# Optimization experiments

Hardware: AMD Instinct MI355X
Metric: run time of the kernel (lower is better)

Reference implementation:

```python
import jax, jax.numpy as jnp
import numpy as np


def _min_gru_layer(h_in, Wz, bz, Wh, bh):
    # h_in: [B, T, D_in]; gates/candidate via two GEMMs
    z = jax.nn.sigmoid(jnp.einsum('btd,dh->bth', h_in, Wz) + bz)  # [B,T,H]
    h_tilde = jnp.einsum('btd,dh->bth', h_in, Wh) + bh            # [B,T,H]
    # Recurrence h_t = a_t * h_{t-1} + b_t with a_t = 1-z_t, b_t = z_t*h_tilde.
    # h_0 = 0 (frozen zeros param in the torch module), so the associative
    # scan over (a, b) directly yields h_t for t = 1..T.
    a = 1.0 - z
    b = z * h_tilde

    def combine(c1, c2):
        a1, b1 = c1
        a2, b2 = c2
        return a1 * a2, a2 * b1 + b2

    _, h = jax.lax.associative_scan(combine, (a, b), axis=1)
    return h


def setup_inputs() -> dict:
    key = jax.random.key(0)
    ks = jax.random.split(key, 8)
    B, T, Din, H, Dout = 8, 4096, 512, 1024, 512
    s_in = 1.0 / np.sqrt(Din)
    s_h = 1.0 / np.sqrt(H)
    return {
        'x':   jax.random.normal(ks[0], (B, T, Din), dtype=jnp.float32),
        'Wz0': jax.random.normal(ks[1], (Din, H), dtype=jnp.float32) * s_in,
        'bz0': jnp.zeros((H,), dtype=jnp.float32),
        'Wh0': jax.random.normal(ks[2], (Din, H), dtype=jnp.float32) * s_in,
        'bh0': jnp.zeros((H,), dtype=jnp.float32),
        'Wz1': jax.random.normal(ks[3], (H, H), dtype=jnp.float32) * s_h,
        'bz1': jnp.zeros((H,), dtype=jnp.float32),
        'Wh1': jax.random.normal(ks[4], (H, H), dtype=jnp.float32) * s_h,
        'bh1': jnp.zeros((H,), dtype=jnp.float32),
        'Wfc': jax.random.normal(ks[5], (H, Dout), dtype=jnp.float32) * s_h,
        'bfc': jnp.zeros((Dout,), dtype=jnp.float32),
    }


def reference(x, Wz0, bz0, Wh0, bh0, Wz1, bz1, Wh1, bh1, Wfc, bfc):
    h = _min_gru_layer(x, Wz0, bz0, Wh0, bh0)   # layer 0
    h = _min_gru_layer(h, Wz1, bz1, Wh1, bh1)   # layer 1
    return jnp.einsum('bth,ho->bto', h, Wfc) + bfc
```

## Files before the change

### kernel.cpp

```cpp
#include <hip/hip_runtime.h>

typedef __attribute__((ext_vector_type(4))) float fv4;
typedef __attribute__((ext_vector_type(8))) _Float16 hv8;
typedef __attribute__((ext_vector_type(4))) _Float16 hv4;
typedef __attribute__((ext_vector_type(2))) _Float16 hv2;

__device__ __forceinline__ void gload16(const void* g, void* l) {
  __builtin_amdgcn_global_load_lds(
      (const __attribute__((address_space(1))) unsigned int*)g,
      (__attribute__((address_space(3))) unsigned int*)l, 16, 0, 0);
}

struct GemmCore256 {
  const _Float16 *ap, *bp;
  size_t rstep;
  _Float16* ls;
  const _Float16 *fa, *fb;
  int wv;

  __device__ __forceinline__ void init(const _Float16* A, const _Float16* Bt,
                                       _Float16* lds, int m0, int n0, int K,
                                       int tid) {
    ls = lds;
    wv = tid >> 6;
    const int lane = tid & 63;
    const int wm = wv >> 2, wn = wv & 3;
    const int quad = lane >> 4, r = lane & 15;
    const int cg = (tid & 3) ^ ((tid >> 3) & 3);
    ap = A  + (size_t)(m0 + (tid >> 2)) * K + cg * 8;
    bp = Bt + (size_t)(n0 + (tid >> 2)) * K + cg * 8;
    rstep = (size_t)128 * K;
    const int sq = quad ^ ((r >> 1) & 3);
    fa = ls + (wm * 128 + r) * 32 + sq * 8;
    fb = ls + 8192 + (wn * 64 + r) * 32 + sq * 8;
  }

  __device__ __forceinline__ void stage(int s) {
    _Float16* d = ls + (s & 3) * 16384 + wv * 512;
    const _Float16* a = ap + (size_t)s * 32;
    const _Float16* b = bp + (size_t)s * 32;
    gload16(a,         d);
    gload16(a + rstep, d + 4096);
    gload16(b,         d + 8192);
    gload16(b + rstep, d + 12288);
  }

  template <int VM>
  __device__ __forceinline__ void body(fv4 acc[8][4], int s) {
    asm volatile("s_waitcnt vmcnt(%0)" :: "n"(VM) : "memory");
    __builtin_amdgcn_s_barrier();
    __builtin_amdgcn_sched_barrier(0);
    const _Float16* fA = fa + (s & 3) * 16384;
    const _Float16* fB = fb + (s & 3) * 16384;
    hv8 a0[4], b0[4], a1[4];
#pragma unroll
    for (int t = 0; t < 4; ++t) a0[t] = *(const hv8*)(fA + t * 512);
#pragma unroll
    for (int t = 0; t < 4; ++t) b0[t] = *(const hv8*)(fB + t * 512);
#pragma unroll
    for (int t = 0; t < 4; ++t) a1[t] = *(const hv8*)(fA + (t + 4) * 512);
    __builtin_amdgcn_s_setprio(1);
#pragma unroll
    for (int tm = 0; tm < 4; ++tm)
#pragma unroll
      for (int tn = 0; tn < 4; ++tn)
        acc[tm][tn] = __builtin_amdgcn_mfma_f32_16x16x32_f16(a0[tm], b0[tn],
                                                             acc[tm][tn], 0, 0, 0);
#pragma unroll
    for (int tm = 0; tm < 4; ++tm)
#pragma unroll
      for (int tn = 0; tn < 4; ++tn)
        acc[tm + 4][tn] = __builtin_amdgcn_mfma_f32_16x16x32_f16(a1[tm], b0[tn],
                                                                 acc[tm + 4][tn], 0, 0, 0);
    __builtin_amdgcn_s_setprio(0);
    asm volatile("s_waitcnt lgkmcnt(0)" ::: "memory");
    __builtin_amdgcn_sched_barrier(0);
    __builtin_amdgcn_s_barrier();
  }

  __device__ __forceinline__ void run(fv4 acc[8][4], int K) {
    const int ns = K >> 5;
    stage(0); stage(1); stage(2);
    int s = 0;
    for (; s < ns - 3; ++s) { stage(s + 3); body<12>(acc, s); }
    body<8>(acc, s); ++s;
    body<4>(acc, s); ++s;
    body<0>(acc, s);
  }
};

__device__ __forceinline__ void xcd_map(int bid, int ntl2, int mt_per_x,
                                        int& m0, int& n0) {
  const int xcd = bid & 7;
  const int k2  = bid >> 3;
  m0 = (xcd * mt_per_x + (k2 >> ntl2)) * 256;
  n0 = (k2 & ((1 << ntl2) - 1)) * 256;
}

__global__ __launch_bounds__(512)
void gemm_gate(const _Float16* __restrict__ A, const _Float16* __restrict__ Btf,
               _Float16* __restrict__ zh2,
               float* __restrict__ cA, float* __restrict__ cB,
               const float* __restrict__ bz, const float* __restrict__ bh,
               int K, int ntl2, int mt_per_x) {
  __shared__ _Float16 lds[4 * 16384];
  const int tid  = threadIdx.x;
  const int lane = tid & 63;
  const int wave = tid >> 6;
  const int wm = wave >> 2, wn = wave & 3;
  const int quad = lane >> 4, r = lane & 15;
  int m0, n0;
  xcd_map(blockIdx.x, ntl2, mt_per_x, m0, n0);

  GemmCore256 core;
  core.init(A, Btf, lds, m0, n0, K, tid);
  fv4 acc[8][4] = {};
  core.run(acc, K);

  const int jb   = (n0 + wn * 64) >> 1;
  const int row0 = m0 + wm * 128 + quad * 4;
  const int cb   = (m0 >> 6) + wm * 2;
#pragma unroll
  for (int tn = 0; tn < 2; ++tn) {
    const int j = jb + tn * 16 + r;
    const float bzv = bz[j];
    const float bhv = bh[j];
#pragma unroll
    for (int tg = 0; tg < 2; ++tg) {
      float qA[4], qB[4];
#pragma unroll
      for (int tq = 0; tq < 4; ++tq) {
        const int tm = tg * 4 + tq;
        float sA = 1.0f, sB = 0.0f;
#pragma unroll
        for (int r2 = 0; r2 < 4; ++r2) {
          const float zpre = acc[tm][tn][r2] + bzv;
          const float hpre = acc[tm][tn + 2][r2] + bhv;
          const float z = 1.0f / (1.0f + __expf(-zpre));
          const _Float16 a16 = (_Float16)(1.0f - z);
          const _Float16 b16 = (_Float16)(z * hpre);
          hv2 ab = {a16, b16};
          *(hv2*)(zh2 + ((size_t)(row0 + tm * 16 + r2) * 1024 + j) * 2) = ab;
          const float af = (float)a16, bf = (float)b16;
          sB = af * sB + bf;
          sA = sA * af;
        }
        qA[tq] = sA; qB[tq] = sB;
      }
#pragma unroll
      for (int tq = 0; tq < 4; ++tq) {
        float Av = qA[tq], Bv = qB[tq];
        float Ap = __shfl_up(Av, 16, 64);
        float Bp = __shfl_up(Bv, 16, 64);
        if (quad >= 1) { Bv = Av * Bp + Bv; Av = Ap * Av; }
        Ap = __shfl_up(Av, 32, 64);
        Bp = __shfl_up(Bv, 32, 64);
        if (quad >= 2) { Bv = Av * Bp + Bv; Av = Ap * Av; }
        qA[tq] = Av; qB[tq] = Bv;
      }
      if (quad == 3) {
        float CA = 1.0f, CB = 0.0f;
#pragma unroll
        for (int tq = 0; tq < 4; ++tq) { CB = qA[tq] * CB + qB[tq]; CA *= qA[tq]; }
        cA[(size_t)(cb + tg) * 1024 + j] = CA;
        cB[(size_t)(cb + tg) * 1024 + j] = CB;
      }
    }
  }
}

__global__ __launch_bounds__(512)
void gemm_f16_bt(const _Float16* __restrict__ A, const _Float16* __restrict__ Bt,
                 float* __restrict__ C, const float* __restrict__ bias,
                 int N, int K, int ntl2, int mt_per_x) {
  __shared__ _Float16 lds[4 * 16384];
  const int tid  = threadIdx.x;
  const int lane = tid & 63;
  const int wave = tid >> 6;
  const int wm = wave >> 2, wn = wave & 3;
  const int quad = lane >> 4, r = lane & 15;
  int m0, n0;
  xcd_map(blockIdx.x, ntl2, mt_per_x, m0, n0);

  GemmCore256 core;
  core.init(A, Bt, lds, m0, n0, K, tid);
  fv4 acc[8][4] = {};
  core.run(acc, K);

  const int col0 = n0 + wn * 64 + r;
  const int row0 = m0 + wm * 128 + quad * 4;
#pragma unroll
  for (int tn = 0; tn < 4; ++tn) {
    const int col = col0 + tn * 16;
    const float bs = bias[col];
#pragma unroll
    for (int tm = 0; tm < 8; ++tm) {
#pragma unroll
      for (int r2 = 0; r2 < 4; ++r2) {
        C[(size_t)(row0 + tm * 16 + r2) * N + col] = acc[tm][tn][r2] + bs;
      }
    }
  }
}

__global__ void cvt_f16(const float* __restrict__ x, _Float16* __restrict__ y) {
  size_t i = ((size_t)blockIdx.x * 256 + threadIdx.x) * 4;
  fv4 v = *(const fv4*)(x + i);
  *(hv4*)(y + i) = __builtin_convertvector(v, hv4);
}

__global__ void transpose_cvt(const float* __restrict__ W, _Float16* __restrict__ Wt,
                              int K, int N, int mult, int off) {
  __shared__ float tile[32][33];
  const int tx = threadIdx.x, ty = threadIdx.y;
  const int n  = blockIdx.x * 32 + tx;
  const int kb = blockIdx.y * 32;
  for (int i = ty; i < 32; i += 8)
    tile[i][tx] = W[(size_t)(kb + i) * N + n];
  __syncthreads();
  const int k = kb + tx;
  for (int i = ty; i < 32; i += 8)
    Wt[(size_t)(blockIdx.x * mult + off + i) * K + k] = (_Float16)tile[tx][i];
}

__global__ void scan_phaseB(const float* __restrict__ cA, const float* __restrict__ cB,
                            float* __restrict__ hcy) {
  const int gtid = blockIdx.x * 256 + threadIdx.x;
  const int lane = gtid & 63;
  const int wid  = gtid >> 6;
  const int h  = (wid & 255) * 4;
  const int bb = wid >> 8;
  const size_t o = (size_t)(bb * 64 + lane) * 1024 + h;
  fv4 Aa = *(const fv4*)(cA + o);
  fv4 Bv = *(const fv4*)(cB + o);
#pragma unroll
  for (int d = 1; d < 64; d <<= 1) {
    fv4 Ap, Bp;
#pragma unroll
    for (int k = 0; k < 4; ++k) {
      Ap[k] = __shfl_up(Aa[k], d, 64);
      Bp[k] = __shfl_up(Bv[k], d, 64);
    }
    if (lane >= d) {
      Bv = Aa * Bp + Bv;
      Aa = Ap * Aa;
    }
  }
  fv4 hc;
#pragma unroll
  for (int k = 0; k < 4; ++k) hc[k] = __shfl_up(Bv[k], 1, 64);
  if (lane == 0) { hc.x = 0.f; hc.y = 0.f; hc.z = 0.f; hc.w = 0.f; }
  *(fv4*)(hcy + o) = hc;
}

__global__ void scan_phaseC(const _Float16* __restrict__ zh2,
                            const float* __restrict__ hcy,
                            _Float16* __restrict__ hout) {
  const int idx = blockIdx.x * 256 + threadIdx.x;
  const int h  = (idx & 255) * 4;
  const int c  = (idx >> 8) & 63;
  const int bb = idx >> 14;
  const size_t base = ((size_t)(bb * 4096 + c * 64) * 1024 + h) * 2;
  const size_t ob   = (size_t)(bb * 4096 + c * 64) * 1024 + h;
  const size_t o    = (size_t)(bb * 64 + c) * 1024 + h;
  fv4 hc = *(const fv4*)(hcy + o);
#pragma unroll 4
  for (int t = 0; t < 64; ++t) {
    hv8 v = *(const hv8*)(zh2 + base + (size_t)t * 2048);
    fv4 av = __builtin_convertvector(__builtin_shufflevector(v, v, 0, 2, 4, 6), fv4);
    fv4 bv = __builtin_convertvector(__builtin_shufflevector(v, v, 1, 3, 5, 7), fv4);
    hc = av * hc + bv;
    *(hv4*)(hout + ob + (size_t)t * 1024) = __builtin_convertvector(hc, hv4);
  }
}

extern "C" void kernel_launch(void* const* d_in, const int* in_sizes, int n_in,
                              void* d_out, int out_size, void* d_ws, size_t ws_size,
                              hipStream_t stream) {
  const float* x   = (const float*)d_in[0];
  const float* Wz0 = (const float*)d_in[1];
  const float* bz0 = (const float*)d_in[2];
  const float* Wh0 = (const float*)d_in[3];
  const float* bh0 = (const float*)d_in[4];
  const float* Wz1 = (const float*)d_in[5];
  const float* bz1 = (const float*)d_in[6];
  const float* Wh1 = (const float*)d_in[7];
  const float* bh1 = (const float*)d_in[8];
  const float* Wfc = (const float*)d_in[9];
  const float* bfc = (const float*)d_in[10];

  const int Mrows = 32768;
  const int H = 1024, Din = 512, Dout = 512;

  char* w = (char*)d_ws;
  _Float16* zh2   = (_Float16*)w; w += (size_t)Mrows * 2 * H * 2;
  _Float16* hx    = (_Float16*)w; w += (size_t)Mrows * H * 2;
  _Float16* Wzh0t = (_Float16*)w; w += (size_t)2 * H * Din * 2;
  _Float16* Wzh1t = (_Float16*)w; w += (size_t)2 * H * H * 2;
  _Float16* Wft   = (_Float16*)w; w += (size_t)Dout * H * 2;
  float*    cA    = (float*)w;    w += (size_t)8 * 64 * H * 4;
  float*    cB    = (float*)w;    w += (size_t)8 * 64 * H * 4;
  float*    hcy   = (float*)w;    w += (size_t)8 * 64 * H * 4;
  _Float16* Xb    = hx;

  cvt_f16<<<Mrows * Din / 1024, 256, 0, stream>>>(x, Xb);
  transpose_cvt<<<dim3(H / 32, Din / 32), dim3(32, 8), 0, stream>>>(Wz0, Wzh0t, Din, H, 64, 0);
  transpose_cvt<<<dim3(H / 32, Din / 32), dim3(32, 8), 0, stream>>>(Wh0, Wzh0t, Din, H, 64, 32);
  transpose_cvt<<<dim3(H / 32, H / 32),   dim3(32, 8), 0, stream>>>(Wz1, Wzh1t, H, H, 64, 0);
  transpose_cvt<<<dim3(H / 32, H / 32),   dim3(32, 8), 0, stream>>>(Wh1, Wzh1t, H, H, 64, 32);
  transpose_cvt<<<dim3(Dout / 32, H / 32), dim3(32, 8), 0, stream>>>(Wfc, Wft, H, Dout, 32, 0);

  gemm_gate<<<1024, 512, 0, stream>>>(Xb, Wzh0t, zh2, cA, cB, bz0, bh0, Din, 3, 16);
  scan_phaseB<<<512, 256, 0, stream>>>(cA, cB, hcy);
  scan_phaseC<<<512, 256, 0, stream>>>(zh2, hcy, hx);

  gemm_gate<<<1024, 512, 0, stream>>>(hx, Wzh1t, zh2, cA, cB, bz1, bh1, H, 3, 16);
  scan_phaseB<<<512, 256, 0, stream>>>(cA, cB, hcy);
  scan_phaseC<<<512, 256, 0, stream>>>(zh2, hcy, hx);

  gemm_f16_bt<<<256, 512, 0, stream>>>(hx, Wft, (float*)d_out, bfc, Dout, H, 1, 16);
}
```

Measured before the change: 506.6 us.

## Split GEMM main loop into two phases with interleaved A/B staging

The per-stage GEMM body is split into two half-phases. Each half reads its LDS fragments, issues global-to-LDS loads for one operand (A or B) of stage s+3, then runs 16 MFMAs, with a barrier and lgkmcnt wait between them. The aim is to spread global loads and LDS reads across the MFMA work and shorten barrier stalls. Both GEMM kernels also get launch_bounds(512, 2) to ask for two blocks per CU. That caps register use while each thread already holds 128 fp32 accumulators, so spills are likely. The 128 KB LDS buffer per block may also stop a second block from fitting at all.

```diff
diff --git a/kernel.cpp b/kernel.cpp
--- a/kernel.cpp
+++ b/kernel.cpp
@@ -35,7 +35,7 @@
     fb = ls + 8192 + (wn * 64 + r) * 32 + sq * 8;
   }
 
-  __device__ __forceinline__ void stage(int s) {
+  __device__ __forceinline__ void stage4(int s) {
     _Float16* d = ls + (s & 3) * 16384 + wv * 512;
     const _Float16* a = ap + (size_t)s * 32;
     const _Float16* b = bp + (size_t)s * 32;
@@ -44,21 +44,33 @@
     gload16(b,         d + 8192);
     gload16(b + rstep, d + 12288);
   }
-
-  template <int VM>
-  __device__ __forceinline__ void body(fv4 acc[8][4], int s) {
-    asm volatile("s_waitcnt vmcnt(%0)" :: "n"(VM) : "memory");
-    __builtin_amdgcn_s_barrier();
-    __builtin_amdgcn_sched_barrier(0);
+  __device__ __forceinline__ void stageA(int s) {
+    _Float16* d = ls + (s & 3) * 16384 + wv * 512;
+    const _Float16* a = ap + (size_t)s * 32;
+    gload16(a,         d);
+    gload16(a + rstep, d + 4096);
+  }
+  __device__ __forceinline__ void stageB(int s) {
+    _Float16* d = ls + (s & 3) * 16384 + wv * 512;
+    const _Float16* b = bp + (size_t)s * 32;
+    gload16(b,         d + 8192);
+    gload16(b + rstep, d + 12288);
+  }
+
+  template <bool STAGE>
+  __device__ __forceinline__ void phaseA(fv4 acc[8][4], hv8 b0[4], int s) {
     const _Float16* fA = fa + (s & 3) * 16384;
     const _Float16* fB = fb + (s & 3) * 16384;
-    hv8 a0[4], b0[4], a1[4];
+    hv8 a0[4];
 #pragma unroll
     for (int t = 0; t < 4; ++t) a0[t] = *(const hv8*)(fA + t * 512);
 #pragma unroll
     for (int t = 0; t < 4; ++t) b0[t] = *(const hv8*)(fB + t * 512);
-#pragma unroll
-    for (int t = 0; t < 4; ++t) a1[t] = *(const hv8*)(fA + (t + 4) * 512);
+    if (STAGE) stageA(s + 3);
+    __builtin_amdgcn_sched_barrier(0);
+    __builtin_amdgcn_s_barrier();
+    asm volatile("s_waitcnt lgkmcnt(0)" ::: "memory");
+    __builtin_amdgcn_sched_barrier(0);
     __builtin_amdgcn_s_setprio(1);
 #pragma unroll
     for (int tm = 0; tm < 4; ++tm)
@@ -66,6 +78,25 @@
       for (int tn = 0; tn < 4; ++tn)
         acc[tm][tn] = __builtin_amdgcn_mfma_f32_16x16x32_f16(a0[tm], b0[tn],
                                                              acc[tm][tn], 0, 0, 0);
+    __builtin_amdgcn_s_setprio(0);
+    __builtin_amdgcn_sched_barrier(0);
+    __builtin_amdgcn_s_barrier();
+  }
+
+  template <int VM, bool STAGE>
+  __device__ __forceinline__ void phaseB(fv4 acc[8][4], hv8 b0[4], int s) {
+    const _Float16* fA = fa + (s & 3) * 16384;
+    hv8 a1[4];
+#pragma unroll
+    for (int t = 0; t < 4; ++t) a1[t] = *(const hv8*)(fA + (t + 4) * 512);
+    if (STAGE) stageB(s + 3);
+    if constexpr (VM >= 0)
+      asm volatile("s_waitcnt vmcnt(%0)" :: "n"(VM) : "memory");
+    __builtin_amdgcn_sched_barrier(0);
+    __builtin_amdgcn_s_barrier();
+    asm volatile("s_waitcnt lgkmcnt(0)" ::: "memory");
+    __builtin_amdgcn_sched_barrier(0);
+    __builtin_amdgcn_s_setprio(1);
 #pragma unroll
     for (int tm = 0; tm < 4; ++tm)
 #pragma unroll
@@ -73,19 +104,24 @@
         acc[tm + 4][tn] = __builtin_amdgcn_mfma_f32_16x16x32_f16(a1[tm], b0[tn],
                                                                  acc[tm + 4][tn], 0, 0, 0);
     __builtin_amdgcn_s_setprio(0);
-    asm volatile("s_waitcnt lgkmcnt(0)" ::: "memory");
     __builtin_amdgcn_sched_barrier(0);
     __builtin_amdgcn_s_barrier();
   }
 
   __device__ __forceinline__ void run(fv4 acc[8][4], int K) {
     const int ns = K >> 5;
-    stage(0); stage(1); stage(2);
+    stage4(0); stage4(1); stage4(2);
+    asm volatile("s_waitcnt vmcnt(8)" ::: "memory");
+    __builtin_amdgcn_s_barrier();
     int s = 0;
-    for (; s < ns - 3; ++s) { stage(s + 3); body<12>(acc, s); }
-    body<8>(acc, s); ++s;
-    body<4>(acc, s); ++s;
-    body<0>(acc, s);
+    for (; s < ns - 3; ++s) {
+      hv8 b0[4];
+      phaseA<true>(acc, b0, s);
+      phaseB<8, true>(acc, b0, s);
+    }
+    { hv8 b0[4]; phaseA<false>(acc, b0, s); phaseB<4, false>(acc, b0, s); } ++s;
+    { hv8 b0[4]; phaseA<false>(acc, b0, s); phaseB<0, false>(acc, b0, s); } ++s;
+    { hv8 b0[4]; phaseA<false>(acc, b0, s); phaseB<-1, false>(acc, b0, s); }
   }
 };
 
@@ -97,7 +133,7 @@
   n0 = (k2 & ((1 << ntl2) - 1)) * 256;
 }
 
-__global__ __launch_bounds__(512)
+__global__ __launch_bounds__(512, 2)
 void gemm_gate(const _Float16* __restrict__ A, const _Float16* __restrict__ Btf,
                _Float16* __restrict__ zh2,
                float* __restrict__ cA, float* __restrict__ cB,
@@ -169,7 +205,7 @@
   }
 }
 
-__global__ __launch_bounds__(512)
+__global__ __launch_bounds__(512, 2)
 void gemm_f16_bt(const _Float16* __restrict__ A, const _Float16* __restrict__ Bt,
                  float* __restrict__ C, const float* __restrict__ bias,
                  int N, int K, int ntl2, int mt_per_x) {
```

Measured after the change: 517.2 us. 1.02x slower.

## Restructure GEMM main loop to one barrier per k-step and add occupancy bound

Applied to the files above, without the earlier changes.

The k-loop of the shared GEMM core now uses a single workgroup barrier per step instead of two. The next stage's global-to-LDS loads are issued right after that barrier, and the vmcnt wait moves to the end of the step. The trailing lgkmcnt wait and second barrier are dropped, so waves can move into the next step sooner and load issue overlaps more with MFMA work. Both GEMM kernels also get __launch_bounds__(512, 2), which caps registers per thread. With a 128-float accumulator per thread, that cap risks spills, and the 128 KB LDS footprint per block may stop two blocks from ever sharing a CU.

```diff
diff --git a/kernel.cpp b/kernel.cpp
--- a/kernel.cpp
+++ b/kernel.cpp
@@ -35,7 +35,7 @@
     fb = ls + 8192 + (wn * 64 + r) * 32 + sq * 8;
   }
 
-  __device__ __forceinline__ void stage(int s) {
+  __device__ __forceinline__ void stage4(int s) {
     _Float16* d = ls + (s & 3) * 16384 + wv * 512;
     const _Float16* a = ap + (size_t)s * 32;
     const _Float16* b = bp + (size_t)s * 32;
@@ -45,20 +45,20 @@
     gload16(b + rstep, d + 12288);
   }
 
-  template <int VM>
+  template <int VM, bool STAGE>
   __device__ __forceinline__ void body(fv4 acc[8][4], int s) {
-    asm volatile("s_waitcnt vmcnt(%0)" :: "n"(VM) : "memory");
     __builtin_amdgcn_s_barrier();
     __builtin_amdgcn_sched_barrier(0);
+    if (STAGE) stage4(s + 3);
     const _Float16* fA = fa + (s & 3) * 16384;
     const _Float16* fB = fb + (s & 3) * 16384;
-    hv8 a0[4], b0[4], a1[4];
+    hv8 a0[8], b0[4];
 #pragma unroll
     for (int t = 0; t < 4; ++t) a0[t] = *(const hv8*)(fA + t * 512);
 #pragma unroll
     for (int t = 0; t < 4; ++t) b0[t] = *(const hv8*)(fB + t * 512);
 #pragma unroll
-    for (int t = 0; t < 4; ++t) a1[t] = *(const hv8*)(fA + (t + 4) * 512);
+    for (int t = 0; t < 4; ++t) a0[t + 4] = *(const hv8*)(fA + (t + 4) * 512);
     __builtin_amdgcn_s_setprio(1);
 #pragma unroll
     for (int tm = 0; tm < 4; ++tm)
@@ -70,22 +70,22 @@
     for (int tm = 0; tm < 4; ++tm)
 #pragma unroll
       for (int tn = 0; tn < 4; ++tn)
-        acc[tm + 4][tn] = __builtin_amdgcn_mfma_f32_16x16x32_f16(a1[tm], b0[tn],
+        acc[tm + 4][tn] = __builtin_amdgcn_mfma_f32_16x16x32_f16(a0[tm + 4], b0[tn],
                                                                  acc[tm + 4][tn], 0, 0, 0);
     __builtin_amdgcn_s_setprio(0);
-    asm volatile("s_waitcnt lgkmcnt(0)" ::: "memory");
-    __builtin_amdgcn_sched_barrier(0);
-    __builtin_amdgcn_s_barrier();
+    if constexpr (VM >= 0)
+      asm volatile("s_waitcnt vmcnt(%0)" :: "n"(VM) : "memory");
   }
 
   __device__ __forceinline__ void run(fv4 acc[8][4], int K) {
     const int ns = K >> 5;
-    stage(0); stage(1); stage(2);
+    stage4(0); stage4(1); stage4(2);
+    asm volatile("s_waitcnt vmcnt(8)" ::: "memory");
     int s = 0;
-    for (; s < ns - 3; ++s) { stage(s + 3); body<12>(acc, s); }
-    body<8>(acc, s); ++s;
-    body<4>(acc, s); ++s;
-    body<0>(acc, s);
+    for (; s < ns - 3; ++s) body<8, true>(acc, s);
+    body<4, false>(acc, s); ++s;
+    body<0, false>(acc, s); ++s;
+    body<-1, false>(acc, s);
   }
 };
 
@@ -97,7 +97,7 @@
   n0 = (k2 & ((1 << ntl2) - 1)) * 256;
 }
 
-__global__ __launch_bounds__(512)
+__global__ __launch_bounds__(512, 2)
 void gemm_gate(const _Float16* __restrict__ A, const _Float16* __restrict__ Btf,
                _Float16* __restrict__ zh2,
                float* __restrict__ cA, float* __restrict__ cB,
@@ -169,7 +169,7 @@
   }
 }
 
-__global__ __launch_bounds__(512)
+__global__ __launch_bounds__(512, 2)
 void gemm_f16_bt(const _Float16* __restrict__ A, const _Float16* __restrict__ Bt,
                  float* __restrict__ C, const float* __restrict__ bias,
                  int N, int K, int ntl2, int mt_per_x) {
```

After: 503.8 us. No clear change (-0.6%).
